# Optimization experiments

Hardware: AMD Instinct MI355X
Metric: run time of the kernel (lower is better)

The kernel has to match this reference:

```python
import jax, jax.numpy as jnp
import numpy as np

B, ENC, DEC, H, W = 8, 64, 128, 128, 128
NEG = -1e30  # masked-softmax fill


def _neighbors(x):
    """x: [B,H,W,C] -> [B,H,W,9,C] 3x3 neighborhood gather (zeros at borders)."""
    b, h, w, c = x.shape
    p = jnp.pad(x, ((0, 0), (1, 1), (1, 1), (0, 0)))
    return jnp.stack([p[:, r:r + h, c_:c_ + w, :] for r in range(3) for c_ in range(3)], axis=3)


def _neighbor_mask(h, w):
    """[H,W,9] bool: which of the 9 neighbors are in-bounds per pixel."""
    m = jnp.pad(jnp.ones((h, w), dtype=bool), ((1, 1), (1, 1)))
    return jnp.stack([m[r:r + h, c_:c_ + w] for r in range(3) for c_ in range(3)], axis=2)


def setup_inputs() -> dict:
    key = jax.random.key(0)
    ks = jax.random.split(key, 12)
    s = 0.05
    return {
        "encoder_features": jax.random.normal(ks[0], (B, ENC, H, W), jnp.float32),
        "decoder_features": jax.random.normal(ks[1], (B, DEC, H, W), jnp.float32),
        "W_enc": jax.random.normal(ks[2], (ENC, ENC), jnp.float32) * s,
        "b_enc": jax.random.normal(ks[3], (ENC,), jnp.float32) * s,
        "W_dec": jax.random.normal(ks[4], (DEC, ENC), jnp.float32) * s,
        "b_dec": jax.random.normal(ks[5], (ENC,), jnp.float32) * s,
        "W_agg": jax.random.normal(ks[6], (ENC, 1), jnp.float32) * s,
        "b_agg": jax.random.normal(ks[7], (1,), jnp.float32) * s,
        "W_attn": jax.random.normal(ks[8], (2 * ENC, ENC), jnp.float32) * s,
        "b_attn": jax.random.normal(ks[9], (ENC,), jnp.float32) * s,
        "conv_w": jax.random.normal(ks[10], (3, 3, DEC, ENC), jnp.float32) * s,  # HWIO
        "conv_b": jax.random.normal(ks[11], (ENC,), jnp.float32) * s,
    }


def reference(encoder_features, decoder_features, W_enc, b_enc, W_dec, b_dec,
              W_agg, b_agg, W_attn, b_attn, conv_w, conv_b):
    # NCHW -> NHWC (format_linear)
    enc = jnp.transpose(encoder_features, (0, 2, 3, 1))  # [B,H,W,ENC]
    dec = jnp.transpose(decoder_features, (0, 2, 3, 1))  # [B,H,W,DEC]

    q = dec @ W_dec + b_dec  # [B,H,W,ENC]
    k = enc @ W_enc + b_enc  # [B,H,W,ENC]
    vals = jax.lax.conv_general_dilated(
        dec, conv_w, window_strides=(1, 1), padding='SAME',
        dimension_numbers=('NHWC', 'HWIO', 'NHWC')) + conv_b  # [B,H,W,ENC]

    kn = _neighbors(k)    # [B,H,W,9,ENC]
    en = _neighbors(enc)  # [B,H,W,9,ENC]
    mask = _neighbor_mask(q.shape[1], q.shape[2])  # [H,W,9]

    # per-neighbor additive score: agg_encoder(tanh(query + key)) -> scalar
    scores = jnp.squeeze(jnp.tanh(q[:, :, :, None, :] + kn) @ W_agg, -1) + b_agg  # [B,H,W,9]
    scores = jnp.where(mask, scores, NEG)
    attn_w = jax.nn.softmax(scores, axis=-1)  # softmax over valid neighbors only
    attn_vec = jnp.einsum('bhwn,bhwnc->bhwc', attn_w, en)  # weighted sum of raw encoder feats

    cat = jnp.concatenate([vals, attn_vec], axis=-1)  # [B,H,W,2*ENC]
    out = cat @ W_attn + b_attn
    out = jnp.where(out >= 0, out, 0.2 * out)  # LeakyReLU(0.2)
    return jnp.transpose(out, (0, 3, 1, 2))  # back to NCHW
```

## Files before the change

kernel.cpp:

```cpp
#include <hip/hip_runtime.h>

#define BB 8
#define ENC_C 64
#define DEC_C 128
#define HH 128
#define WW 128

typedef unsigned short ushort_t;
typedef __attribute__((ext_vector_type(8))) short short8;
typedef __attribute__((ext_vector_type(4))) short short4v;
typedef __attribute__((ext_vector_type(4))) float f32x4;

static __device__ __forceinline__ ushort_t f2bf(float x) {
  unsigned int u = __builtin_bit_cast(unsigned int, x);
  u += 0x7fff + ((u >> 16) & 1);
  return (ushort_t)(u >> 16);
}
static __device__ __forceinline__ float bf2f(ushort_t v) {
  unsigned int u = ((unsigned int)v) << 16;
  return __builtin_bit_cast(float, u);
}

__global__ __launch_bounds__(64) void pack_w_kernel(
    const float* __restrict__ conv_w, const float* __restrict__ W_attn,
    const float* __restrict__ W_dec, const float* __restrict__ W_enc,
    const float* __restrict__ conv_b, const float* __restrict__ b_attn,
    ushort_t* __restrict__ packedC2, ushort_t* __restrict__ packedW2,
    ushort_t* __restrict__ packedQ, ushort_t* __restrict__ packedK,
    float* __restrict__ bias_total)
{
  const int blk = blockIdx.x;
  const int l = threadIdx.x;

  if (blk < 144) {
    const int kstep = blk >> 2, nf = blk & 3;
    const int tap = kstep >> 2, dstep = kstep & 3;
    const int n = nf * 16 + (l & 15);
    const int dbase = dstep * 32 + (l >> 4) * 8;
    float wcol[64];
    #pragma unroll
    for (int c = 0; c < 64; ++c) wcol[c] = W_attn[c * 64 + n];
    ushort_t v[8];
    #pragma unroll
    for (int j = 0; j < 8; ++j) {
      const float* cw = conv_w + ((long)(tap * DEC_C + dbase + j)) * 64;
      float acc = 0.f;
      #pragma unroll
      for (int c = 0; c < 64; ++c) acc = __builtin_fmaf(cw[c], wcol[c], acc);
      v[j] = f2bf(acc);
    }
    ushort_t* d = packedC2 + (((long)tap * 16 + dstep * 4 + nf) * 64 + l) * 8;
    #pragma unroll
    for (int j = 0; j < 8; ++j) d[j] = v[j];
    return;
  }
  if (blk == 176) {
    float acc = b_attn[l];
    #pragma unroll
    for (int c = 0; c < 64; ++c)
      acc = __builtin_fmaf(conv_b[c], W_attn[c * 64 + l], acc);
    bias_total[l] = acc;
    return;
  }

  const float* W;
  ushort_t* dst;
  int bb, krow0;
  if (blk < 152)      { W = W_attn; dst = packedW2; bb = blk - 144; krow0 = 64; }
  else if (blk < 168) { W = W_dec;  dst = packedQ;  bb = blk - 152; krow0 = 0; }
  else                { W = W_enc;  dst = packedK;  bb = blk - 168; krow0 = 0; }
  const int ks = bb >> 2, nf = bb & 3;
  const int n = nf * 16 + (l & 15);
  const int kbase = krow0 + ks * 32 + (l >> 4) * 8;
  ushort_t v[8];
  #pragma unroll
  for (int j = 0; j < 8; ++j)
    v[j] = f2bf(W[(kbase + j) * 64 + n]);
  ushort_t* d = dst + ((long)bb * 64 + l) * 8;
  #pragma unroll
  for (int j = 0; j < 8; ++j) d[j] = v[j];
}

__global__ __launch_bounds__(256) void prep_kernel(
    const float* __restrict__ enc, const float* __restrict__ dec,
    const ushort_t* __restrict__ packedQ, const ushort_t* __restrict__ packedK,
    const ushort_t* __restrict__ packedW2,
    const float* __restrict__ b_enc, const float* __restrict__ b_dec,
    ushort_t* __restrict__ q_nhwc, ushort_t* __restrict__ k_nhwc,
    ushort_t* __restrict__ encw, ushort_t* __restrict__ dec_t)
{
  __shared__ float smem[WW * 68];
  const int bh = blockIdx.x;
  const int b = bh >> 7, h = bh & 127;
  const int tid = threadIdx.x;
  const int l = tid & 63;
  const int wv = tid >> 6;
  const int pix0 = wv * 32;
  const int col = l & 15, kg = l >> 4;
  const long plane = (long)HH * WW;

  {
    const float* ebase = enc + ((long)(b * ENC_C) * HH + h) * WW;
    f32x4 acck[2][4], accw[2][4];
    #pragma unroll
    for (int mf = 0; mf < 2; ++mf)
      #pragma unroll
      for (int nf = 0; nf < 4; ++nf) {
        acck[mf][nf] = (f32x4){0.f, 0.f, 0.f, 0.f};
        accw[mf][nf] = (f32x4){0.f, 0.f, 0.f, 0.f};
      }

    #pragma unroll
    for (int ks = 0; ks < 2; ++ks) {
      short8 afr[2];
      #pragma unroll
      for (int mf = 0; mf < 2; ++mf) {
        const int pix = pix0 + mf * 16 + col;
        const float* p = ebase + (long)(ks * 32 + kg * 8) * plane + pix;
        short8 v;
        #pragma unroll
        for (int j = 0; j < 8; ++j) v[j] = (short)f2bf(p[(long)j * plane]);
        afr[mf] = v;
      }
      #pragma unroll
      for (int nf = 0; nf < 4; ++nf) {
        const short8 bk =
            *(const short8*)(packedK + ((long)(ks * 4 + nf) * 64 + l) * 8);
        const short8 bw =
            *(const short8*)(packedW2 + ((long)(ks * 4 + nf) * 64 + l) * 8);
        #pragma unroll
        for (int mf = 0; mf < 2; ++mf) {
          acck[mf][nf] = __builtin_amdgcn_mfma_f32_16x16x32_bf16(
              afr[mf], bk, acck[mf][nf], 0, 0, 0);
          accw[mf][nf] = __builtin_amdgcn_mfma_f32_16x16x32_bf16(
              afr[mf], bw, accw[mf][nf], 0, 0, 0);
        }
      }
    }
    #pragma unroll
    for (int mf = 0; mf < 2; ++mf)
      #pragma unroll
      for (int nf = 0; nf < 4; ++nf)
        #pragma unroll
        for (int r = 0; r < 4; ++r) {
          const int pix = pix0 + mf * 16 + kg * 4 + r;
          const int c = nf * 16 + col;
          k_nhwc[((long)bh * WW + pix) * 64 + c] =
              f2bf(acck[mf][nf][r] + b_enc[c]);
          encw[((long)bh * WW + pix) * 64 + c] = f2bf(accw[mf][nf][r]);
        }
  }

  f32x4 accq[2][4];
  #pragma unroll
  for (int mf = 0; mf < 2; ++mf)
    #pragma unroll
    for (int nf = 0; nf < 4; ++nf)
      accq[mf][nf] = (f32x4){0.f, 0.f, 0.f, 0.f};

  #pragma unroll
  for (int hf = 0; hf < 2; ++hf) {
    {
      const int w = tid & 127;
      const int cq = tid >> 7;
      const float* dbase =
          dec + ((long)(b * DEC_C + hf * 64) * HH + h) * WW + w;
      #pragma unroll
      for (int i = 0; i < 8; ++i) {
        const int cb4 = (i * 2 + cq) * 4;
        float4 v;
        v.x = dbase[(long)(cb4 + 0) * plane];
        v.y = dbase[(long)(cb4 + 1) * plane];
        v.z = dbase[(long)(cb4 + 2) * plane];
        v.w = dbase[(long)(cb4 + 3) * plane];
        *(float4*)&smem[w * 68 + cb4] = v;
      }
    }
    __syncthreads();

    #pragma unroll
    for (int i = 0; i < 8; ++i) {
      const int idx = tid + i * 256;
      const int wl = idx >> 4;
      const int cq4 = (idx & 15) * 4;
      const float4 v = *(const float4*)&smem[wl * 68 + cq4];
      short4v s;
      s[0] = (short)f2bf(v.x); s[1] = (short)f2bf(v.y);
      s[2] = (short)f2bf(v.z); s[3] = (short)f2bf(v.w);
      *(short4v*)(dec_t + ((long)bh * WW + wl) * DEC_C + hf * 64 + cq4) = s;
    }

    #pragma unroll
    for (int ks2 = 0; ks2 < 2; ++ks2) {
      const int ks = hf * 2 + ks2;
      short8 afr[2];
      #pragma unroll
      for (int mf = 0; mf < 2; ++mf) {
        const int pix = pix0 + mf * 16 + col;
        const float4* p = (const float4*)&smem[pix * 68 + ks2 * 32 + kg * 8];
        float4 x0 = p[0], x1 = p[1];
        short8 v;
        v[0] = (short)f2bf(x0.x); v[1] = (short)f2bf(x0.y);
        v[2] = (short)f2bf(x0.z); v[3] = (short)f2bf(x0.w);
        v[4] = (short)f2bf(x1.x); v[5] = (short)f2bf(x1.y);
        v[6] = (short)f2bf(x1.z); v[7] = (short)f2bf(x1.w);
        afr[mf] = v;
      }
      #pragma unroll
      for (int nf = 0; nf < 4; ++nf) {
        const short8 bfr =
            *(const short8*)(packedQ + ((long)(ks * 4 + nf) * 64 + l) * 8);
        accq[0][nf] = __builtin_amdgcn_mfma_f32_16x16x32_bf16(
            afr[0], bfr, accq[0][nf], 0, 0, 0);
        accq[1][nf] = __builtin_amdgcn_mfma_f32_16x16x32_bf16(
            afr[1], bfr, accq[1][nf], 0, 0, 0);
      }
    }
    __syncthreads();
  }

  #pragma unroll
  for (int mf = 0; mf < 2; ++mf)
    #pragma unroll
    for (int nf = 0; nf < 4; ++nf)
      #pragma unroll
      for (int r = 0; r < 4; ++r) {
        const int pix = pix0 + mf * 16 + kg * 4 + r;
        const int c = nf * 16 + col;
        q_nhwc[((long)bh * WW + pix) * 64 + c] = f2bf(accq[mf][nf][r] + b_dec[c]);
      }
}

__global__ __launch_bounds__(256) void attn_kernel(
    const ushort_t* __restrict__ q_nhwc, const ushort_t* __restrict__ k_nhwc,
    const ushort_t* __restrict__ encw, const float* __restrict__ W_agg,
    const float* __restrict__ b_agg, ushort_t* __restrict__ attw2)
{
  const int nwg = gridDim.x;
  const int cpx = nwg >> 3;
  const int bid = blockIdx.x;
  const int swz = (bid & 7) * cpx + (bid >> 3);
  const int t = swz * 256 + threadIdx.x;
  const int pix = t >> 2;
  const int cb = (t & 3) * 16;
  const int h = (pix >> 7) & 127;
  const int w = pix & 127;

  int off[9]; bool valid[9];
  #pragma unroll
  for (int n = 0; n < 9; ++n) {
    const int dh = n / 3 - 1, dw = n % 3 - 1;
    const int nh = h + dh, nw = w + dw;
    valid[n] = (nh >= 0 && nh < HH && nw >= 0 && nw < WW);
    const int nhc = min(max(nh, 0), HH - 1);
    const int nwc = min(max(nw, 0), WW - 1);
    off[n] = (pix & ~16383) + nhc * WW + nwc;
  }

  const short8* qp = (const short8*)(q_nhwc + ((long)pix << 6) + cb);
  const short8 qa = qp[0], qb = qp[1];

  float wa[16];
  {
    float4 w0 = *(const float4*)(W_agg + cb);
    float4 w1 = *(const float4*)(W_agg + cb + 4);
    float4 w2 = *(const float4*)(W_agg + cb + 8);
    float4 w3 = *(const float4*)(W_agg + cb + 12);
    wa[0]=w0.x; wa[1]=w0.y; wa[2]=w0.z; wa[3]=w0.w;
    wa[4]=w1.x; wa[5]=w1.y; wa[6]=w1.z; wa[7]=w1.w;
    wa[8]=w2.x; wa[9]=w2.y; wa[10]=w2.z; wa[11]=w2.w;
    wa[12]=w3.x; wa[13]=w3.y; wa[14]=w3.z; wa[15]=w3.w;
  }

  float s[9];
  #pragma unroll
  for (int n = 0; n < 9; ++n) {
    const short8* kp = (const short8*)(k_nhwc + ((long)off[n] << 6) + cb);
    const short8 ka = kp[0], kb = kp[1];
    float sc = 0.f;
    #pragma unroll
    for (int e = 0; e < 8; ++e) {
      float x = bf2f((ushort_t)qa[e]) + bf2f((ushort_t)ka[e]);
      x = fminf(fmaxf(x, -15.f), 15.f);
      float z = __builtin_amdgcn_exp2f(x * 2.88539008f);
      float tt = __builtin_fmaf(-2.f, __builtin_amdgcn_rcpf(z + 1.f), 1.f);
      sc = __builtin_fmaf(tt, wa[e], sc);
    }
    #pragma unroll
    for (int e = 0; e < 8; ++e) {
      float x = bf2f((ushort_t)qb[e]) + bf2f((ushort_t)kb[e]);
      x = fminf(fmaxf(x, -15.f), 15.f);
      float z = __builtin_amdgcn_exp2f(x * 2.88539008f);
      float tt = __builtin_fmaf(-2.f, __builtin_amdgcn_rcpf(z + 1.f), 1.f);
      sc = __builtin_fmaf(tt, wa[8 + e], sc);
    }
    s[n] = sc;
  }

  #pragma unroll
  for (int n = 0; n < 9; ++n) {
    s[n] += __shfl_xor(s[n], 1);
    s[n] += __shfl_xor(s[n], 2);
  }

  const float bagg = b_agg[0];
  float m = -1e30f;
  #pragma unroll
  for (int n = 0; n < 9; ++n) {
    s[n] = valid[n] ? (s[n] + bagg) : -1e30f;
    m = fmaxf(m, s[n]);
  }
  float attw[9]; float denom = 0.f;
  #pragma unroll
  for (int n = 0; n < 9; ++n) {
    attw[n] = __builtin_amdgcn_exp2f((s[n] - m) * 1.44269504f);
    denom += attw[n];
  }
  const float inv = __builtin_amdgcn_rcpf(denom);
  #pragma unroll
  for (int n = 0; n < 9; ++n) attw[n] *= inv;

  float a16[16];
  #pragma unroll
  for (int e = 0; e < 16; ++e) a16[e] = 0.f;
  #pragma unroll
  for (int n = 0; n < 9; ++n) {
    const short8* ep = (const short8*)(encw + ((long)off[n] << 6) + cb);
    const short8 ea = ep[0], eb = ep[1];
    #pragma unroll
    for (int e = 0; e < 8; ++e)
      a16[e] = __builtin_fmaf(attw[n], bf2f((ushort_t)ea[e]), a16[e]);
    #pragma unroll
    for (int e = 0; e < 8; ++e)
      a16[8 + e] = __builtin_fmaf(attw[n], bf2f((ushort_t)eb[e]), a16[8 + e]);
  }
  short8 o0, o1;
  #pragma unroll
  for (int e = 0; e < 8; ++e) {
    o0[e] = (short)f2bf(a16[e]);
    o1[e] = (short)f2bf(a16[8 + e]);
  }
  short8* op = (short8*)(attw2 + ((long)pix << 6) + cb);
  op[0] = o0;
  op[1] = o1;
}

__global__ __launch_bounds__(256) void conv2_kernel(
    const ushort_t* __restrict__ dec_t, const ushort_t* __restrict__ packedC2,
    const ushort_t* __restrict__ attw2, const float* __restrict__ bias_total,
    float* __restrict__ out)
{
  __shared__ ushort_t bsh[16384];
  const int nwg = gridDim.x;
  const int cpx = nwg >> 3;
  const int bid = blockIdx.x;
  const int bh = (bid & 7) * cpx + (bid >> 3);
  const int b = bh >> 7, h = bh & 127;
  const int tid = threadIdx.x;
  const int l = tid & 63;
  const int wv = tid >> 6;
  const int pix0 = wv * 32;
  const int col = l & 15, kg = l >> 4;

  auto stage = [&](int tap) {
    const ushort_t* src = packedC2 + (long)tap * 8192;
    ushort_t* dstb = bsh + (tap & 1) * 8192 + (long)(tid & ~63) * 8;
    #pragma unroll
    for (int i = 0; i < 4; ++i) {
      __builtin_amdgcn_global_load_lds(
          (const __attribute__((address_space(1))) void*)(src + (long)(i * 256 + tid) * 8),
          (__attribute__((address_space(3))) void*)(dstb + i * 256 * 8),
          16, 0, 0);
    }
  };

  f32x4 acc[4][2];
  #pragma unroll
  for (int mf = 0; mf < 4; ++mf)
    #pragma unroll
    for (int pf = 0; pf < 2; ++pf)
      acc[mf][pf] = (f32x4){0.f, 0.f, 0.f, 0.f};

  stage(0);

  #pragma unroll
  for (int p = 0; p < 9; ++p) {
    __syncthreads();
    if (p + 1 < 9) stage(p + 1);
    const int kh = p / 3, kw = p % 3;
    const int hh = h + kh - 1;
    if (hh >= 0 && hh < HH) {
      const ushort_t* arow = dec_t + ((long)(b * HH + hh) * WW) * DEC_C;
      const ushort_t* bbase = bsh + (p & 1) * 8192;
      short8 pfr[4][2];
      #pragma unroll
      for (int pf = 0; pf < 2; ++pf) {
        const int wp = pix0 + pf * 16 + col + kw - 1;
        const bool ok = (wp >= 0 && wp < WW);
        #pragma unroll
        for (int ds = 0; ds < 4; ++ds) {
          short8 z = {0, 0, 0, 0, 0, 0, 0, 0};
          pfr[ds][pf] = ok
              ? *(const short8*)(arow + (long)wp * DEC_C + ds * 32 + kg * 8) : z;
        }
      }
      #pragma unroll
      for (int ds = 0; ds < 4; ++ds)
        #pragma unroll
        for (int mf = 0; mf < 4; ++mf) {
          const short8 wfr =
              *(const short8*)(bbase + ((ds * 4 + mf) * 64 + l) * 8);
          acc[mf][0] = __builtin_amdgcn_mfma_f32_16x16x32_bf16(
              wfr, pfr[ds][0], acc[mf][0], 0, 0, 0);
          acc[mf][1] = __builtin_amdgcn_mfma_f32_16x16x32_bf16(
              wfr, pfr[ds][1], acc[mf][1], 0, 0, 0);
        }
    }
  }

  #pragma unroll
  for (int mf = 0; mf < 4; ++mf)
    #pragma unroll
    for (int pf = 0; pf < 2; ++pf) {
      const int pix = pix0 + pf * 16 + col;
      const short4v av = *(const short4v*)(
          attw2 + ((long)bh * WW + pix) * 64 + mf * 16 + kg * 4);
      #pragma unroll
      for (int r = 0; r < 4; ++r) {
        const int ch = mf * 16 + kg * 4 + r;
        float o = acc[mf][pf][r] + bf2f((ushort_t)av[r]) + bias_total[ch];
        o = (o >= 0.f) ? o : 0.2f * o;
        out[((long)(b * ENC_C + ch) * HH + h) * WW + pix] = o;
      }
    }
}

extern "C" void kernel_launch(void* const* d_in, const int* in_sizes, int n_in,
                              void* d_out, int out_size, void* d_ws, size_t ws_size,
                              hipStream_t stream) {
  const float* enc    = (const float*)d_in[0];
  const float* dec    = (const float*)d_in[1];
  const float* W_enc  = (const float*)d_in[2];
  const float* b_enc  = (const float*)d_in[3];
  const float* W_dec  = (const float*)d_in[4];
  const float* b_dec  = (const float*)d_in[5];
  const float* W_agg  = (const float*)d_in[6];
  const float* b_agg  = (const float*)d_in[7];
  const float* W_attn = (const float*)d_in[8];
  const float* b_attn = (const float*)d_in[9];
  const float* conv_w = (const float*)d_in[10];
  const float* conv_b = (const float*)d_in[11];
  float* out = (float*)d_out;

  const long npix = (long)BB * HH * WW;
  ushort_t* q_bf     = (ushort_t*)d_ws;
  ushort_t* k_bf     = q_bf + npix * 64;
  ushort_t* encw     = k_bf + npix * 64;
  ushort_t* dec_t    = encw + npix * 64;
  ushort_t* attw2    = dec_t + npix * 128;
  ushort_t* packedC2 = attw2 + npix * 64;
  ushort_t* packedW2 = packedC2 + 144 * 64 * 8;
  ushort_t* packedQ  = packedW2 + 8 * 64 * 8;
  ushort_t* packedK  = packedQ + 16 * 64 * 8;
  float* bias_total  = (float*)(packedK + 8 * 64 * 8);

  hipLaunchKernelGGL(pack_w_kernel, dim3(177), dim3(64), 0, stream,
                     conv_w, W_attn, W_dec, W_enc, conv_b, b_attn,
                     packedC2, packedW2, packedQ, packedK, bias_total);
  hipLaunchKernelGGL(prep_kernel, dim3(BB * HH), dim3(256), 0, stream,
                     enc, dec, packedQ, packedK, packedW2, b_enc, b_dec,
                     q_bf, k_bf, encw, dec_t);
  hipLaunchKernelGGL(attn_kernel, dim3((int)(npix * 4 / 256)), dim3(256), 0, stream,
                     q_bf, k_bf, encw, W_agg, b_agg, attw2);
  hipLaunchKernelGGL(conv2_kernel, dim3(BB * HH), dim3(256), 0, stream,
                     dec_t, packedC2, attw2, bias_total, out);
}
```

Measured before the change: 136.0 us.

## Split prep kernel per half-row with per-wave LDS staging and no block barriers

The prep kernel now gives each block half an image row (64 pixels), with each wave owning 16 pixels, so the grid doubles and each block needs much less shared memory. Encoder and decoder data are staged through a per-wave LDS slice, so __syncthreads is no longer needed and encoder reads become coalesced instead of strided per-lane gathers. Block IDs are swizzled across groups of eight. The aim is higher occupancy and better memory coalescing, at the cost of less reuse of the weight fragments per wave (one M-tile instead of two).

Measured after the change: 120.5 us. 1.13x faster.

```diff
diff --git a/kernel.cpp b/kernel.cpp
--- a/kernel.cpp
+++ b/kernel.cpp
@@ -89,146 +89,122 @@
     ushort_t* __restrict__ q_nhwc, ushort_t* __restrict__ k_nhwc,
     ushort_t* __restrict__ encw, ushort_t* __restrict__ dec_t)
 {
-  __shared__ float smem[WW * 68];
-  const int bh = blockIdx.x;
-  const int b = bh >> 7, h = bh & 127;
+  __shared__ float smem[4 * 16 * 68];
+  const int nwg = gridDim.x;
+  const int cpx = nwg >> 3;
+  const int bid = blockIdx.x;
+  const int grp = (bid & 7) * cpx + (bid >> 3);
+  const int b = grp >> 8;
+  const int h = (grp & 255) >> 1;
+  const int half = grp & 1;
+  const int bh = b * HH + h;
   const int tid = threadIdx.x;
   const int l = tid & 63;
   const int wv = tid >> 6;
-  const int pix0 = wv * 32;
+  const int pw = half * 64 + wv * 16;
   const int col = l & 15, kg = l >> 4;
   const long plane = (long)HH * WW;
+  float* swl = smem + wv * 16 * 68;
 
   {
-    const float* ebase = enc + ((long)(b * ENC_C) * HH + h) * WW;
-    f32x4 acck[2][4], accw[2][4];
-    #pragma unroll
-    for (int mf = 0; mf < 2; ++mf)
-      #pragma unroll
-      for (int nf = 0; nf < 4; ++nf) {
-        acck[mf][nf] = (f32x4){0.f, 0.f, 0.f, 0.f};
-        accw[mf][nf] = (f32x4){0.f, 0.f, 0.f, 0.f};
-      }
+    const float* ebase = enc + ((long)(b * ENC_C) * HH + h) * WW + pw;
+    #pragma unroll
+    for (int i = 0; i < 16; ++i) {
+      const int cc = i * 4 + kg;
+      swl[col * 68 + cc] = ebase[(long)cc * plane + col];
+    }
+
+    f32x4 acck[4], accw[4];
+    #pragma unroll
+    for (int nf = 0; nf < 4; ++nf) {
+      acck[nf] = (f32x4){0.f, 0.f, 0.f, 0.f};
+      accw[nf] = (f32x4){0.f, 0.f, 0.f, 0.f};
+    }
 
     #pragma unroll
     for (int ks = 0; ks < 2; ++ks) {
-      short8 afr[2];
-      #pragma unroll
-      for (int mf = 0; mf < 2; ++mf) {
-        const int pix = pix0 + mf * 16 + col;
-        const float* p = ebase + (long)(ks * 32 + kg * 8) * plane + pix;
-        short8 v;
-        #pragma unroll
-        for (int j = 0; j < 8; ++j) v[j] = (short)f2bf(p[(long)j * plane]);
-        afr[mf] = v;
-      }
+      const float4* p = (const float4*)&swl[col * 68 + ks * 32 + kg * 8];
+      float4 x0 = p[0], x1 = p[1];
+      short8 afr;
+      afr[0] = (short)f2bf(x0.x); afr[1] = (short)f2bf(x0.y);
+      afr[2] = (short)f2bf(x0.z); afr[3] = (short)f2bf(x0.w);
+      afr[4] = (short)f2bf(x1.x); afr[5] = (short)f2bf(x1.y);
+      afr[6] = (short)f2bf(x1.z); afr[7] = (short)f2bf(x1.w);
       #pragma unroll
       for (int nf = 0; nf < 4; ++nf) {
         const short8 bk =
             *(const short8*)(packedK + ((long)(ks * 4 + nf) * 64 + l) * 8);
         const short8 bw =
             *(const short8*)(packedW2 + ((long)(ks * 4 + nf) * 64 + l) * 8);
-        #pragma unroll
-        for (int mf = 0; mf < 2; ++mf) {
-          acck[mf][nf] = __builtin_amdgcn_mfma_f32_16x16x32_bf16(
-              afr[mf], bk, acck[mf][nf], 0, 0, 0);
-          accw[mf][nf] = __builtin_amdgcn_mfma_f32_16x16x32_bf16(
-              afr[mf], bw, accw[mf][nf], 0, 0, 0);
-        }
+        acck[nf] = __builtin_amdgcn_mfma_f32_16x16x32_bf16(
+            afr, bk, acck[nf], 0, 0, 0);
+        accw[nf] = __builtin_amdgcn_mfma_f32_16x16x32_bf16(
+            afr, bw, accw[nf], 0, 0, 0);
       }
     }
     #pragma unroll
-    for (int mf = 0; mf < 2; ++mf)
-      #pragma unroll
-      for (int nf = 0; nf < 4; ++nf)
-        #pragma unroll
-        for (int r = 0; r < 4; ++r) {
-          const int pix = pix0 + mf * 16 + kg * 4 + r;
-          const int c = nf * 16 + col;
-          k_nhwc[((long)bh * WW + pix) * 64 + c] =
-              f2bf(acck[mf][nf][r] + b_enc[c]);
-          encw[((long)bh * WW + pix) * 64 + c] = f2bf(accw[mf][nf][r]);
-        }
-  }
-
-  f32x4 accq[2][4];
-  #pragma unroll
-  for (int mf = 0; mf < 2; ++mf)
-    #pragma unroll
     for (int nf = 0; nf < 4; ++nf)
-      accq[mf][nf] = (f32x4){0.f, 0.f, 0.f, 0.f};
+      #pragma unroll
+      for (int r = 0; r < 4; ++r) {
+        const int px = pw + kg * 4 + r;
+        const int c = nf * 16 + col;
+        k_nhwc[((long)bh * WW + px) * 64 + c] = f2bf(acck[nf][r] + b_enc[c]);
+        encw[((long)bh * WW + px) * 64 + c] = f2bf(accw[nf][r]);
+      }
+  }
+
+  f32x4 accq[4];
+  #pragma unroll
+  for (int nf = 0; nf < 4; ++nf) accq[nf] = (f32x4){0.f, 0.f, 0.f, 0.f};
 
   #pragma unroll
   for (int hf = 0; hf < 2; ++hf) {
-    {
-      const int w = tid & 127;
-      const int cq = tid >> 7;
-      const float* dbase =
-          dec + ((long)(b * DEC_C + hf * 64) * HH + h) * WW + w;
-      #pragma unroll
-      for (int i = 0; i < 8; ++i) {
-        const int cb4 = (i * 2 + cq) * 4;
-        float4 v;
-        v.x = dbase[(long)(cb4 + 0) * plane];
-        v.y = dbase[(long)(cb4 + 1) * plane];
-        v.z = dbase[(long)(cb4 + 2) * plane];
-        v.w = dbase[(long)(cb4 + 3) * plane];
-        *(float4*)&smem[w * 68 + cb4] = v;
-      }
-    }
-    __syncthreads();
-
-    #pragma unroll
-    for (int i = 0; i < 8; ++i) {
-      const int idx = tid + i * 256;
-      const int wl = idx >> 4;
-      const int cq4 = (idx & 15) * 4;
-      const float4 v = *(const float4*)&smem[wl * 68 + cq4];
+    const float* dbase =
+        dec + ((long)(b * DEC_C + hf * 64) * HH + h) * WW + pw;
+    #pragma unroll
+    for (int i = 0; i < 16; ++i) {
+      const int cc = i * 4 + kg;
+      swl[col * 68 + cc] = dbase[(long)cc * plane + col];
+    }
+
+    #pragma unroll
+    for (int i = 0; i < 4; ++i) {
+      const int px = kg + i * 4;
+      const float4 v = *(const float4*)&swl[px * 68 + col * 4];
       short4v s;
       s[0] = (short)f2bf(v.x); s[1] = (short)f2bf(v.y);
       s[2] = (short)f2bf(v.z); s[3] = (short)f2bf(v.w);
-      *(short4v*)(dec_t + ((long)bh * WW + wl) * DEC_C + hf * 64 + cq4) = s;
+      *(short4v*)(dec_t + ((long)bh * WW + pw + px) * DEC_C + hf * 64 + col * 4) = s;
     }
 
     #pragma unroll
     for (int ks2 = 0; ks2 < 2; ++ks2) {
       const int ks = hf * 2 + ks2;
-      short8 afr[2];
-      #pragma unroll
-      for (int mf = 0; mf < 2; ++mf) {
-        const int pix = pix0 + mf * 16 + col;
-        const float4* p = (const float4*)&smem[pix * 68 + ks2 * 32 + kg * 8];
-        float4 x0 = p[0], x1 = p[1];
-        short8 v;
-        v[0] = (short)f2bf(x0.x); v[1] = (short)f2bf(x0.y);
-        v[2] = (short)f2bf(x0.z); v[3] = (short)f2bf(x0.w);
-        v[4] = (short)f2bf(x1.x); v[5] = (short)f2bf(x1.y);
-        v[6] = (short)f2bf(x1.z); v[7] = (short)f2bf(x1.w);
-        afr[mf] = v;
-      }
+      const float4* p = (const float4*)&swl[col * 68 + ks2 * 32 + kg * 8];
+      float4 x0 = p[0], x1 = p[1];
+      short8 afr;
+      afr[0] = (short)f2bf(x0.x); afr[1] = (short)f2bf(x0.y);
+      afr[2] = (short)f2bf(x0.z); afr[3] = (short)f2bf(x0.w);
+      afr[4] = (short)f2bf(x1.x); afr[5] = (short)f2bf(x1.y);
+      afr[6] = (short)f2bf(x1.z); afr[7] = (short)f2bf(x1.w);
       #pragma unroll
       for (int nf = 0; nf < 4; ++nf) {
         const short8 bfr =
             *(const short8*)(packedQ + ((long)(ks * 4 + nf) * 64 + l) * 8);
-        accq[0][nf] = __builtin_amdgcn_mfma_f32_16x16x32_bf16(
-            afr[0], bfr, accq[0][nf], 0, 0, 0);
-        accq[1][nf] = __builtin_amdgcn_mfma_f32_16x16x32_bf16(
-            afr[1], bfr, accq[1][nf], 0, 0, 0);
+        accq[nf] = __builtin_amdgcn_mfma_f32_16x16x32_bf16(
+            afr, bfr, accq[nf], 0, 0, 0);
       }
     }
-    __syncthreads();
-  }
-
-  #pragma unroll
-  for (int mf = 0; mf < 2; ++mf)
-    #pragma unroll
-    for (int nf = 0; nf < 4; ++nf)
-      #pragma unroll
-      for (int r = 0; r < 4; ++r) {
-        const int pix = pix0 + mf * 16 + kg * 4 + r;
-        const int c = nf * 16 + col;
-        q_nhwc[((long)bh * WW + pix) * 64 + c] = f2bf(accq[mf][nf][r] + b_dec[c]);
-      }
+  }
+
+  #pragma unroll
+  for (int nf = 0; nf < 4; ++nf)
+    #pragma unroll
+    for (int r = 0; r < 4; ++r) {
+      const int px = pw + kg * 4 + r;
+      const int c = nf * 16 + col;
+      q_nhwc[((long)bh * WW + px) * 64 + c] = f2bf(accq[nf][r] + b_dec[c]);
+    }
 }
 
 __global__ __launch_bounds__(256) void attn_kernel(
@@ -467,7 +443,7 @@
   hipLaunchKernelGGL(pack_w_kernel, dim3(177), dim3(64), 0, stream,
                      conv_w, W_attn, W_dec, W_enc, conv_b, b_attn,
                      packedC2, packedW2, packedQ, packedK, bias_total);
-  hipLaunchKernelGGL(prep_kernel, dim3(BB * HH), dim3(256), 0, stream,
+  hipLaunchKernelGGL(prep_kernel, dim3(BB * HH * 2), dim3(256), 0, stream,
                      enc, dec, packedQ, packedK, packedW2, b_enc, b_dec,
                      q_bf, k_bf, encw, dec_t);
   hipLaunchKernelGGL(attn_kernel, dim3((int)(npix * 4 / 256)), dim3(256), 0, stream,
```
